# Performance work log

Measured on AMD Instinct MI355X. Metric: run time of the kernel, lower is better.

The kernel has to match this reference:

```python
import jax, jax.numpy as jnp
import numpy as np

DEPTH = 128
NEG_MAX = -jnp.finfo(jnp.float32).max


def setup_inputs() -> dict:
    key = jax.random.key(0)
    ks = jax.random.split(key, 10)
    B, S, F, C = 16, 2048, 512, 1000
    x = jax.random.normal(ks[0], (B, S, F), dtype=jnp.float32)
    attention_mask = jax.random.randint(ks[1], (B, S, S), 0, 2) == 1
    s = 1.0 / np.sqrt(F)
    Wq = jax.random.uniform(ks[2], (F, DEPTH), jnp.float32, -s, s)
    bq = jax.random.uniform(ks[3], (DEPTH,), jnp.float32, -s, s)
    Wk = jax.random.uniform(ks[4], (F, DEPTH), jnp.float32, -s, s)
    bk = jax.random.uniform(ks[5], (DEPTH,), jnp.float32, -s, s)
    Wv = jax.random.uniform(ks[6], (F, DEPTH), jnp.float32, -s, s)
    bv = jax.random.uniform(ks[7], (DEPTH,), jnp.float32, -s, s)
    sl = 1.0 / np.sqrt(DEPTH)
    Wl = jax.random.uniform(ks[8], (DEPTH, C), jnp.float32, -sl, sl)
    bl = jax.random.uniform(ks[9], (C,), jnp.float32, -sl, sl)
    return {"x": x, "attention_mask": attention_mask,
            "Wq": Wq, "bq": bq, "Wk": Wk, "bk": bk,
            "Wv": Wv, "bv": bv, "Wl": Wl, "bl": bl}


def reference(x, attention_mask, Wq, bq, Wk, bk, Wv, bv, Wl, bl):
    # x: [B, S, F]; single-head attention with depth=128
    q = (x @ Wq + bq) * (DEPTH ** -0.5)          # [B, S, D] (is_scaled_dot_product)
    k = x @ Wk + bk                               # [B, S, D]
    v = x @ Wv + bv                               # [B, S, D]
    logit = jnp.einsum('bsd,btd->bst', q, k)      # [B, S, S]
    # masked_fill_(mask, -float_max) then added to logits
    logit = logit + jnp.where(attention_mask, NEG_MAX, 0.0)
    attn = jax.nn.softmax(logit, axis=2)
    out = jnp.einsum('bst,btd->bsd', attn, v)     # [B, S, D]
    out = out @ Wl + bl                           # [B, S, C]
    return out.mean(axis=1)                       # [B, C]
```

## Files before the change

### kernel.cpp

```cpp
#include <hip/hip_runtime.h>
#include <stdint.h>

#define BB 16
#define SS 2048
#define FF 512
#define DD 128
#define CC 1000

typedef __attribute__((ext_vector_type(8))) short bf16x8;
typedef __attribute__((ext_vector_type(4))) float f32x4;

__device__ __forceinline__ unsigned short f2bf(float f) {
  unsigned x;
  __builtin_memcpy(&x, &f, 4);
  x = x + 0x7FFFu + ((x >> 16) & 1u);
  return (unsigned short)(x >> 16);
}
__device__ __forceinline__ float bf2f(unsigned short u) {
  unsigned x = ((unsigned)u) << 16;
  float f;
  __builtin_memcpy(&f, &x, 4);
  return f;
}
__device__ __forceinline__ unsigned pk2(float a, float b) {
  return (unsigned)f2bf(a) | ((unsigned)f2bf(b) << 16);
}

#define WS_WG   256
#define WS_ZG   131328
#define WS_YG   262400
#define WS_PK   270592
#define WS_Q    8659200
#define WS_K    17047808
#define WS_V    25436416
#define WS_WT   33825024
#define WS_END  34218240

__global__ __launch_bounds__(256) void k_wt(const float* __restrict__ Wq,
                                            const float* __restrict__ Wk,
                                            const float* __restrict__ Wv,
                                            unsigned short* __restrict__ wt,
                                            const unsigned* __restrict__ mask,
                                            int* __restrict__ flags,
                                            float* __restrict__ wgl,
                                            float* __restrict__ zgl,
                                            float* __restrict__ ygl) {
  const int tid = threadIdx.x;
  if (blockIdx.x == 768) {
    __shared__ unsigned red;
    if (tid == 0) red = 0;
    __syncthreads();
    unsigned a = 0;
#pragma unroll
    for (int j = 0; j < 4; ++j) a |= mask[tid * 4 + j] & 0xFFFFFF00u;
    if (a) atomicOr(&red, 1u);
    __syncthreads();
    if (tid == 0) flags[0] = (red == 0) ? 1 : 0;
    for (int i = tid; i < BB * SS; i += 256) { wgl[i] = 0.f; zgl[i] = 0.f; }
    for (int i = tid; i < BB * DD; i += 256) ygl[i] = 0.f;
    return;
  }
  int idx = blockIdx.x * 256 + tid;
  int ty = idx >> 16;
  int o = idx & 65535;
  int d = o >> 9, f = o & 511;
  const float* W = ty == 0 ? Wq : (ty == 1 ? Wk : Wv);
  wt[idx] = f2bf(W[f * DD + d]);
}

__global__ __launch_bounds__(256) void k_pack(const void* __restrict__ mask,
                                              const int* __restrict__ flags,
                                              unsigned* __restrict__ pk) {
  const int tid = threadIdx.x;
  const long long base = (long long)blockIdx.x * 32768;
  const bool isInt = flags[0] != 0;
  for (int it = 0; it < 128; ++it) {
    long long e = base + it * 256 + tid;
    int val;
    if (isInt) val = ((const int*)mask)[e];
    else       val = ((const unsigned char*)mask)[e];
    unsigned long long bal = __ballot(val != 0);
    if ((tid & 31) == 0)
      pk[e >> 5] = (unsigned)((tid & 63) ? (bal >> 32) : bal);
  }
}

__global__ __launch_bounds__(256) void k_proj(const float* __restrict__ xg,
                                              const unsigned short* __restrict__ wtg,
                                              const float* __restrict__ bq,
                                              const float* __restrict__ bk,
                                              const float* __restrict__ bv,
                                              unsigned short* __restrict__ qo,
                                              unsigned short* __restrict__ ko,
                                              unsigned short* __restrict__ vo) {
  __shared__ __align__(16) char lA[8192];
  __shared__ __align__(16) char lB[8192];
  const int tid = threadIdx.x;
  const int lane = tid & 63;
  const int wv = tid >> 6;
  const int colL = lane & 15, quad = lane >> 4;
  const int blk = blockIdx.x, ty = blockIdx.y;
  const float* bias = ty == 0 ? bq : (ty == 1 ? bk : bv);
  unsigned short* outp = ty == 0 ? qo : (ty == 1 ? ko : vo);
  const float scale = ty == 0 ? 0.08838834764831845f : 1.0f;
  const unsigned short* wbase = wtg + (size_t)ty * 65536;
  const int m0 = (wv & 1) * 64, n0 = (wv >> 1) * 64;

  f32x4 acc[4][4];
  const f32x4 z4 = {0.f, 0.f, 0.f, 0.f};
#pragma unroll
  for (int mi = 0; mi < 4; ++mi)
#pragma unroll
    for (int ni = 0; ni < 4; ++ni) acc[mi][ni] = z4;

  for (int ic = 0; ic < 16; ++ic) {
    const int k0 = ic * 32;
    uint4 va[2], vb[2];
#pragma unroll
    for (int rr = 0; rr < 2; ++rr) {
      int p = rr * 256 + tid;
      int row = p >> 2, c = p & 3;
      const float* xp = xg + (size_t)(blk * 128 + row) * FF + k0 + c * 8;
      float4 x0 = *(const float4*)xp;
      float4 x1 = *(const float4*)(xp + 4);
      va[rr].x = pk2(x0.x, x0.y); va[rr].y = pk2(x0.z, x0.w);
      va[rr].z = pk2(x1.x, x1.y); va[rr].w = pk2(x1.z, x1.w);
      vb[rr] = *(const uint4*)(wbase + (size_t)row * FF + k0 + c * 8);
    }
    __syncthreads();
#pragma unroll
    for (int rr = 0; rr < 2; ++rr) {
      int p = rr * 256 + tid;
      int row = p >> 2, c = p & 3;
      int phys = c ^ ((row >> 1) & 3);
      *(uint4*)(lA + row * 64 + phys * 16) = va[rr];
      *(uint4*)(lB + row * 64 + phys * 16) = vb[rr];
    }
    __syncthreads();
    bf16x8 af[4], bfr[4];
#pragma unroll
    for (int mi = 0; mi < 4; ++mi) {
      int ar = m0 + mi * 16 + colL;
      int phys = quad ^ ((ar >> 1) & 3);
      af[mi] = *(const bf16x8*)(lA + ar * 64 + phys * 16);
    }
#pragma unroll
    for (int ni = 0; ni < 4; ++ni) {
      int br = n0 + ni * 16 + colL;
      int phys = quad ^ ((br >> 1) & 3);
      bfr[ni] = *(const bf16x8*)(lB + br * 64 + phys * 16);
    }
#pragma unroll
    for (int mi = 0; mi < 4; ++mi)
#pragma unroll
      for (int ni = 0; ni < 4; ++ni)
        acc[mi][ni] = __builtin_amdgcn_mfma_f32_16x16x32_bf16(af[mi], bfr[ni], acc[mi][ni], 0, 0, 0);
  }
#pragma unroll
  for (int ni = 0; ni < 4; ++ni) {
    int col = n0 + ni * 16 + colL;
    float bval = bias[col];
#pragma unroll
    for (int mi = 0; mi < 4; ++mi) {
#pragma unroll
      for (int r = 0; r < 4; ++r) {
        int row = blk * 128 + m0 + mi * 16 + quad * 4 + r;
        float val = (acc[mi][ni][r] + bval) * scale;
        outp[(size_t)row * DD + col] = f2bf(val);
      }
    }
  }
}

__global__ __launch_bounds__(512, 2) void k_fatt(const unsigned short* __restrict__ qg,
                                                 const unsigned short* __restrict__ kg,
                                                 const unsigned* __restrict__ pk,
                                                 float* __restrict__ wg) {
  extern __shared__ __align__(16) char smem[];
  unsigned short* pt = (unsigned short*)smem;
  char* kt = smem + 131072;
  unsigned* mk = (unsigned*)(smem + 147456);
  float* zfin = (float*)(smem + 155776);
  float* zinvl = (float*)(smem + 155904);

  const int tid = threadIdx.x;
  const int lane = tid & 63, wv = tid >> 6;
  const int colL = lane & 15, quad = lane >> 4;
  const int wr = wv & 1, wq = wv >> 1;
  const int r0 = blockIdx.x * 32;
  const int b = blockIdx.y;

  for (int i = tid; i < 2048; i += 512) {
    int row = i >> 6, w = i & 63;
    mk[row * 65 + w] = pk[((size_t)b * SS + r0 + row) * 64 + w];
  }
  if (tid < 32) zfin[tid] = 0.f;

  bf16x8 qf[4];
  {
    int qrow = r0 + wr * 16 + colL;
    const unsigned short* qp = qg + ((size_t)b * SS + qrow) * DD + quad * 8;
#pragma unroll
    for (int kk = 0; kk < 4; ++kk) qf[kk] = *(const bf16x8*)(qp + kk * 32);
  }

  const int krow = tid >> 3, kc8 = tid & 7;
  const unsigned short* kbase = kg + ((size_t)b * SS + krow) * DD;
  const int kswz0 = (kc8 ^ (krow & 7)) * 16;
  const int kswz1 = ((kc8 + 8) ^ (krow & 7)) * 16;

  uint4 kreg0 = *(const uint4*)(kbase + kc8 * 8);
  uint4 kreg1 = *(const uint4*)(kbase + kc8 * 8 + 64);
  *(uint4*)(kt + krow * 256 + kswz0) = kreg0;
  *(uint4*)(kt + krow * 256 + kswz1) = kreg1;
  __syncthreads();

  float z[4] = {0.f, 0.f, 0.f, 0.f};
  const int tb = wq * 16 + colL;

  for (int c = 0; c < 32; ++c) {
    if (c < 31) {
      const unsigned short* kb2 = kbase + (size_t)(c + 1) * 64 * DD;
      kreg0 = *(const uint4*)(kb2 + kc8 * 8);
      kreg1 = *(const uint4*)(kb2 + kc8 * 8 + 64);
    }
    bf16x8 bb[4];
#pragma unroll
    for (int kk = 0; kk < 4; ++kk) {
      int phys = (kk * 4 + quad) ^ (tb & 7);
      bb[kk] = *(const bf16x8*)(kt + tb * 256 + phys * 16);
    }
    f32x4 acc = {0.f, 0.f, 0.f, 0.f};
    acc = __builtin_amdgcn_mfma_f32_16x16x32_bf16(qf[0], bb[0], acc, 0, 0, 0);
    acc = __builtin_amdgcn_mfma_f32_16x16x32_bf16(qf[1], bb[1], acc, 0, 0, 0);
    acc = __builtin_amdgcn_mfma_f32_16x16x32_bf16(qf[2], bb[2], acc, 0, 0, 0);
    acc = __builtin_amdgcn_mfma_f32_16x16x32_bf16(qf[3], bb[3], acc, 0, 0, 0);
    int tl = c * 64 + tb;
    int widx = tl >> 5, wb = tl & 31;
#pragma unroll
    for (int r = 0; r < 4; ++r) {
      int row_l = wr * 16 + quad * 4 + r;
      unsigned mw = mk[row_l * 65 + widx];
      float e = ((mw >> wb) & 1u) ? 0.f : __expf(fminf(acc[r], 80.f));
      z[r] += e;
      pt[row_l * 2048 + (tl ^ ((row_l & 7) << 3))] = f2bf(e);
    }
    if (c < 31) {
      __syncthreads();
      *(uint4*)(kt + krow * 256 + kswz0) = kreg0;
      *(uint4*)(kt + krow * 256 + kswz1) = kreg1;
      __syncthreads();
    }
  }

#pragma unroll
  for (int r = 0; r < 4; ++r) {
    float s = z[r];
    s += __shfl_xor(s, 1, 64);
    s += __shfl_xor(s, 2, 64);
    s += __shfl_xor(s, 4, 64);
    s += __shfl_xor(s, 8, 64);
    if (colL == 0) atomicAdd(&zfin[wr * 16 + quad * 4 + r], s);
  }
  __syncthreads();
  if (tid < 32) zinvl[tid] = 1.0f / fmaxf(zfin[tid], 1e-30f);
  __syncthreads();

  {
    const int t0 = tid * 4;
    float a0 = 0.f, a1 = 0.f, a2 = 0.f, a3 = 0.f;
#pragma unroll 8
    for (int r = 0; r < 32; ++r) {
      const unsigned short* pr = pt + r * 2048 + (t0 ^ ((r & 7) << 3));
      ushort4 pv = *(const ushort4*)pr;
      float zi = zinvl[r];
      a0 += bf2f(pv.x) * zi;
      a1 += bf2f(pv.y) * zi;
      a2 += bf2f(pv.z) * zi;
      a3 += bf2f(pv.w) * zi;
    }
    float* wrow = wg + (size_t)b * SS + t0;
    atomicAdd(&wrow[0], a0);
    atomicAdd(&wrow[1], a1);
    atomicAdd(&wrow[2], a2);
    atomicAdd(&wrow[3], a3);
  }
}

__global__ __launch_bounds__(256) void k_yv(const float* __restrict__ wgl,
                                            const unsigned short* __restrict__ vg,
                                            float* __restrict__ ygl) {
  const int tid = threadIdx.x;
  const int tc = blockIdx.x, b = blockIdx.y;
  const int d = tid & 127, half = tid >> 7;
  const int t0 = tc * 128 + half * 64;
  float p = 0.f;
  const float* wrow = wgl + (size_t)b * SS + t0;
  const unsigned short* vrow = vg + ((size_t)b * SS + t0) * DD + d;
#pragma unroll 8
  for (int t = 0; t < 64; ++t) p += wrow[t] * bf2f(vrow[(size_t)t * DD]);
  atomicAdd(&ygl[b * DD + d], p);
}

__global__ __launch_bounds__(256) void k_out(const float* __restrict__ ygl,
                                             const float* __restrict__ Wl,
                                             const float* __restrict__ bl,
                                             float* __restrict__ outp) {
  __shared__ float ys[DD];
  const int tid = threadIdx.x;
  const int b = blockIdx.x;
  if (tid < DD) ys[tid] = ygl[b * DD + tid] * (1.0f / 2048.0f);
  __syncthreads();
  for (int c = tid; c < CC; c += 256) {
    float a = bl[c];
#pragma unroll 16
    for (int dd = 0; dd < DD; ++dd) a += ys[dd] * Wl[dd * CC + c];
    outp[b * CC + c] = a;
  }
}

extern "C" void kernel_launch(void* const* d_in, const int* in_sizes, int n_in,
                              void* d_out, int out_size, void* d_ws, size_t ws_size,
                              hipStream_t stream) {
  const void* ptr[10];
  for (int i = 0; i < 10; ++i) ptr[i] = (i < n_in) ? d_in[i] : nullptr;
  if (n_in == 10) {
    const void *px = 0, *pm = 0, *pWl = 0, *pbl = 0;
    const void* pW[3] = {0, 0, 0};
    const void* pb[3] = {0, 0, 0};
    int nW = 0, nb = 0;
    for (int i = 0; i < 10; ++i) {
      int s = in_sizes[i];
      if (s == 16777216) px = d_in[i];
      else if (s == 67108864) pm = d_in[i];
      else if (s == 128000) pWl = d_in[i];
      else if (s == 1000) pbl = d_in[i];
      else if (s == 65536 && nW < 3) pW[nW++] = d_in[i];
      else if (s == 128 && nb < 3) pb[nb++] = d_in[i];
    }
    if (px && pm && pWl && pbl && nW == 3 && nb == 3) {
      ptr[0] = px; ptr[1] = pm;
      ptr[2] = pW[0]; ptr[3] = pb[0];
      ptr[4] = pW[1]; ptr[5] = pb[1];
      ptr[6] = pW[2]; ptr[7] = pb[2];
      ptr[8] = pWl; ptr[9] = pbl;
    }
  }
  char* ws = (char*)d_ws;
  if (ws_size < (size_t)WS_END) return;
  int* flags = (int*)ws;
  float* wg = (float*)(ws + WS_WG);
  float* zg = (float*)(ws + WS_ZG);
  float* yg = (float*)(ws + WS_YG);
  unsigned* pk = (unsigned*)(ws + WS_PK);
  unsigned short* q  = (unsigned short*)(ws + WS_Q);
  unsigned short* k  = (unsigned short*)(ws + WS_K);
  unsigned short* v  = (unsigned short*)(ws + WS_V);
  unsigned short* wt = (unsigned short*)(ws + WS_WT);

  k_wt<<<769, 256, 0, stream>>>((const float*)ptr[2], (const float*)ptr[4],
                                (const float*)ptr[6], wt,
                                (const unsigned*)ptr[1], flags, wg, zg, yg);
  k_pack<<<2048, 256, 0, stream>>>(ptr[1], flags, pk);
  k_proj<<<dim3(256, 3), 256, 0, stream>>>((const float*)ptr[0], wt,
                                           (const float*)ptr[3], (const float*)ptr[5],
                                           (const float*)ptr[7], q, k, v);
  k_fatt<<<dim3(64, 16), 512, 156032, stream>>>(q, k, pk, wg);
  k_yv<<<dim3(16, 16), 256, 0, stream>>>(wg, v, yg);
  k_out<<<16, 256, 0, stream>>>(yg, (const float*)ptr[8], (const float*)ptr[9],
                                (float*)d_out);
}
```

Before: 610.9 us.

## Fuse prep kernels, replace atomics with partial buffers, merge tail kernels

Merges the weight-transpose and mask-packing kernels into one prep kernel, with each block detecting the mask format on its own. The attention kernel now writes per-row-block partial column sums to a workspace buffer instead of issuing atomicAdds, so the zeroing pass is no longer needed. A single 1024-thread tail kernel per batch reduces the partials, applies V and then the output linear layer, replacing two kernels. This cuts launch count, atomics and zero-init work, at the cost of a larger workspace and a tail that runs on only 16 blocks.

Result: faster. 577.3 us (median of 2 runs) (-5.5%).

```diff
diff --git a/kernel.cpp b/kernel.cpp
--- a/kernel.cpp
+++ b/kernel.cpp
@@ -26,54 +26,35 @@
   return (unsigned)f2bf(a) | ((unsigned)f2bf(b) << 16);
 }
 
-#define WS_WG   256
-#define WS_ZG   131328
-#define WS_YG   262400
-#define WS_PK   270592
-#define WS_Q    8659200
-#define WS_K    17047808
-#define WS_V    25436416
-#define WS_WT   33825024
-#define WS_END  34218240
-
-__global__ __launch_bounds__(256) void k_wt(const float* __restrict__ Wq,
-                                            const float* __restrict__ Wk,
-                                            const float* __restrict__ Wv,
-                                            unsigned short* __restrict__ wt,
-                                            const unsigned* __restrict__ mask,
-                                            int* __restrict__ flags,
-                                            float* __restrict__ wgl,
-                                            float* __restrict__ zgl,
-                                            float* __restrict__ ygl) {
+#define WS_PK   0
+#define WS_Q    8388608
+#define WS_K    16777216
+#define WS_V    25165824
+#define WS_WT   33554432
+#define WS_WGP  33947648
+#define WS_END  42336256
+
+__global__ __launch_bounds__(256) void k_prep(const void* __restrict__ mask,
+                                              const float* __restrict__ Wq,
+                                              const float* __restrict__ Wk,
+                                              const float* __restrict__ Wv,
+                                              unsigned short* __restrict__ wt,
+                                              unsigned* __restrict__ pk) {
+  __shared__ unsigned red;
   const int tid = threadIdx.x;
-  if (blockIdx.x == 768) {
-    __shared__ unsigned red;
-    if (tid == 0) red = 0;
-    __syncthreads();
+  if (tid == 0) red = 0;
+  __syncthreads();
+  {
     unsigned a = 0;
-#pragma unroll
-    for (int j = 0; j < 4; ++j) a |= mask[tid * 4 + j] & 0xFFFFFF00u;
+    const unsigned* m32 = (const unsigned*)mask;
+#pragma unroll
+    for (int j = 0; j < 4; ++j) a |= m32[tid * 4 + j] & 0xFFFFFF00u;
     if (a) atomicOr(&red, 1u);
-    __syncthreads();
-    if (tid == 0) flags[0] = (red == 0) ? 1 : 0;
-    for (int i = tid; i < BB * SS; i += 256) { wgl[i] = 0.f; zgl[i] = 0.f; }
-    for (int i = tid; i < BB * DD; i += 256) ygl[i] = 0.f;
-    return;
-  }
-  int idx = blockIdx.x * 256 + tid;
-  int ty = idx >> 16;
-  int o = idx & 65535;
-  int d = o >> 9, f = o & 511;
-  const float* W = ty == 0 ? Wq : (ty == 1 ? Wk : Wv);
-  wt[idx] = f2bf(W[f * DD + d]);
-}
-
-__global__ __launch_bounds__(256) void k_pack(const void* __restrict__ mask,
-                                              const int* __restrict__ flags,
-                                              unsigned* __restrict__ pk) {
-  const int tid = threadIdx.x;
+  }
+  __syncthreads();
+  const bool isInt = (red == 0);
+
   const long long base = (long long)blockIdx.x * 32768;
-  const bool isInt = flags[0] != 0;
   for (int it = 0; it < 128; ++it) {
     long long e = base + it * 256 + tid;
     int val;
@@ -82,6 +63,15 @@
     unsigned long long bal = __ballot(val != 0);
     if ((tid & 31) == 0)
       pk[e >> 5] = (unsigned)((tid & 63) ? (bal >> 32) : bal);
+  }
+
+  if (blockIdx.x < 768) {
+    int idx = blockIdx.x * 256 + tid;
+    int ty = idx >> 16;
+    int o = idx & 65535;
+    int d = o >> 9, f = o & 511;
+    const float* W = ty == 0 ? Wq : (ty == 1 ? Wk : Wv);
+    wt[idx] = f2bf(W[f * DD + d]);
   }
 }
 
@@ -175,7 +165,7 @@
 __global__ __launch_bounds__(512, 2) void k_fatt(const unsigned short* __restrict__ qg,
                                                  const unsigned short* __restrict__ kg,
                                                  const unsigned* __restrict__ pk,
-                                                 float* __restrict__ wg) {
+                                                 float* __restrict__ wgp) {
   extern __shared__ __align__(16) char smem[];
   unsigned short* pt = (unsigned short*)smem;
   char* kt = smem + 131072;
@@ -279,43 +269,59 @@
       a2 += bf2f(pv.z) * zi;
       a3 += bf2f(pv.w) * zi;
     }
-    float* wrow = wg + (size_t)b * SS + t0;
-    atomicAdd(&wrow[0], a0);
-    atomicAdd(&wrow[1], a1);
-    atomicAdd(&wrow[2], a2);
-    atomicAdd(&wrow[3], a3);
-  }
-}
-
-__global__ __launch_bounds__(256) void k_yv(const float* __restrict__ wgl,
-                                            const unsigned short* __restrict__ vg,
-                                            float* __restrict__ ygl) {
-  const int tid = threadIdx.x;
-  const int tc = blockIdx.x, b = blockIdx.y;
-  const int d = tid & 127, half = tid >> 7;
-  const int t0 = tc * 128 + half * 64;
-  float p = 0.f;
-  const float* wrow = wgl + (size_t)b * SS + t0;
-  const unsigned short* vrow = vg + ((size_t)b * SS + t0) * DD + d;
-#pragma unroll 8
-  for (int t = 0; t < 64; ++t) p += wrow[t] * bf2f(vrow[(size_t)t * DD]);
-  atomicAdd(&ygl[b * DD + d], p);
-}
-
-__global__ __launch_bounds__(256) void k_out(const float* __restrict__ ygl,
-                                             const float* __restrict__ Wl,
-                                             const float* __restrict__ bl,
-                                             float* __restrict__ outp) {
-  __shared__ float ys[DD];
+    float4 o4;
+    o4.x = a0; o4.y = a1; o4.z = a2; o4.w = a3;
+    *(float4*)(wgp + ((size_t)b * 64 + blockIdx.x) * SS + t0) = o4;
+  }
+}
+
+__global__ __launch_bounds__(1024) void k_tail(const float* __restrict__ wgp,
+                                               const unsigned short* __restrict__ vg,
+                                               const float* __restrict__ Wl,
+                                               const float* __restrict__ bl,
+                                               float* __restrict__ outp) {
+  __shared__ float ws2[2048];
+  __shared__ float yp[8][128];
+  __shared__ float ys[128];
   const int tid = threadIdx.x;
   const int b = blockIdx.x;
-  if (tid < DD) ys[tid] = ygl[b * DD + tid] * (1.0f / 2048.0f);
-  __syncthreads();
-  for (int c = tid; c < CC; c += 256) {
-    float a = bl[c];
+
+  {
+    float s0 = 0.f, s1 = 0.f;
+    const float* wp = wgp + ((size_t)b * 64) * SS + tid * 2;
+#pragma unroll 8
+    for (int rg = 0; rg < 64; ++rg) {
+      s0 += wp[rg * SS];
+      s1 += wp[rg * SS + 1];
+    }
+    ws2[tid * 2] = s0;
+    ws2[tid * 2 + 1] = s1;
+  }
+  __syncthreads();
+
+  {
+    const int d = tid & 127, tg = tid >> 7;
+    const int t0 = tg * 256;
+    float p = 0.f;
+    const unsigned short* vr = vg + ((size_t)b * SS + t0) * DD + d;
+#pragma unroll 8
+    for (int t = 0; t < 256; ++t) p += ws2[t0 + t] * bf2f(vr[(size_t)t * DD]);
+    yp[tg][d] = p;
+  }
+  __syncthreads();
+  if (tid < 128) {
+    float a = 0.f;
+#pragma unroll
+    for (int g = 0; g < 8; ++g) a += yp[g][tid];
+    ys[tid] = a * (1.0f / 2048.0f);
+  }
+  __syncthreads();
+
+  if (tid < CC) {
+    float a = bl[tid];
 #pragma unroll 16
-    for (int dd = 0; dd < DD; ++dd) a += ys[dd] * Wl[dd * CC + c];
-    outp[b * CC + c] = a;
+    for (int dd = 0; dd < DD; ++dd) a += ys[dd] * Wl[dd * CC + tid];
+    outp[b * CC + tid] = a;
   }
 }
 
@@ -348,25 +354,19 @@
   }
   char* ws = (char*)d_ws;
   if (ws_size < (size_t)WS_END) return;
-  int* flags = (int*)ws;
-  float* wg = (float*)(ws + WS_WG);
-  float* zg = (float*)(ws + WS_ZG);
-  float* yg = (float*)(ws + WS_YG);
   unsigned* pk = (unsigned*)(ws + WS_PK);
   unsigned short* q  = (unsigned short*)(ws + WS_Q);
   unsigned short* k  = (unsigned short*)(ws + WS_K);
   unsigned short* v  = (unsigned short*)(ws + WS_V);
   unsigned short* wt = (unsigned short*)(ws + WS_WT);
-
-  k_wt<<<769, 256, 0, stream>>>((const float*)ptr[2], (const float*)ptr[4],
-                                (const float*)ptr[6], wt,
-                                (const unsigned*)ptr[1], flags, wg, zg, yg);
-  k_pack<<<2048, 256, 0, stream>>>(ptr[1], flags, pk);
+  float* wgp = (float*)(ws + WS_WGP);
+
+  k_prep<<<2048, 256, 0, stream>>>(ptr[1], (const float*)ptr[2], (const float*)ptr[4],
+                                   (const float*)ptr[6], wt, pk);
   k_proj<<<dim3(256, 3), 256, 0, stream>>>((const float*)ptr[0], wt,
                                            (const float*)ptr[3], (const float*)ptr[5],
                                            (const float*)ptr[7], q, k, v);
-  k_fatt<<<dim3(64, 16), 512, 156032, stream>>>(q, k, pk, wg);
-  k_yv<<<dim3(16, 16), 256, 0, stream>>>(wg, v, yg);
-  k_out<<<16, 256, 0, stream>>>(yg, (const float*)ptr[8], (const float*)ptr[9],
-                                (float*)d_out);
-}
+  k_fatt<<<dim3(64, 16), 512, 156032, stream>>>(q, k, pk, wgp);
+  k_tail<<<16, 1024, 0, stream>>>(wgp, v, (const float*)ptr[8], (const float*)ptr[9],
+                                  (float*)d_out);
+}
```
